# Kernel optimization log

Measured on AMD Instinct MI355X. Metric: run time of the kernel, lower is better.

The kernel has to match this reference:

```python
import jax, jax.numpy as jnp
import numpy as np

RADIUS = 5
KERNEL_SIZE = 2 * RADIUS - 1  # 9
PAD = KERNEL_SIZE // 2        # 4
H, W = 2048, 2048


def make_distance_kernel():
    center = RADIUS - 1
    y, x = jnp.meshgrid(jnp.arange(KERNEL_SIZE), jnp.arange(KERNEL_SIZE), indexing='ij')
    d = jnp.sqrt((x - center).astype(jnp.float32) ** 2 + (y - center).astype(jnp.float32) ** 2)
    return d.at[center, center].set(0.0)


def setup_inputs() -> dict:
    key = jax.random.key(0)
    target = (jax.random.uniform(key, (5, H, W)) < 0.15).astype(jnp.float32)
    distance_kernel = make_distance_kernel()
    return {"target": target, "distance_kernel": distance_kernel}


def _contour_weights(target, kernel):
    combined = (target.sum(axis=0) > 0).astype(jnp.float32)          # [H, W]
    padded = jnp.pad(combined, PAD, mode='edge')                      # replicate pad
    min_d = jnp.full_like(combined, jnp.inf)
    inf = jnp.float32(jnp.inf)
    for i in range(KERNEL_SIZE):
        for j in range(KERNEL_SIZE):
            if i == PAD and j == PAD:
                continue
            shifted = padded[i:i + H, j:j + W]
            diff = (shifted != combined).astype(jnp.float32)
            dist = jnp.where(diff > 0, kernel[i, j] / (diff + 1e-10), inf)
            min_d = jnp.minimum(min_d, dist)
    return jnp.where(min_d < inf, 1.0 / (min_d + 1e-10), 0.0)


def reference(target, distance_kernel):
    feature_weight = target.sum(axis=0)                               # [H, W]
    contour = _contour_weights(target, distance_kernel)
    weights = (feature_weight + contour) ** 2
    weights = (weights - weights.min()) / (weights.max() - weights.min() + 1e-10)
    return weights * (target.sum(axis=0) > 0).astype(jnp.float32)
```

## Files before the change

### kernel.cpp

```cpp
#include <hip/hip_runtime.h>
#include <stdint.h>

#define HH 2048
#define WW 2048
#define NPIX (HH*WW)
#define TS 64
#define NBX (WW/TS)
#define NBY (HH/TS)
#define NBLK (NBX*NBY)
#define HR (TS+8)
#define QW 18
#define BST 24
#define MW 3

__global__ __launch_bounds__(512, 2) void fused_kernel(
    const float* __restrict__ target, const float* __restrict__ dk,
    uint8_t* __restrict__ wcode, float* __restrict__ pmin, float* __restrict__ pmax)
{
    __shared__ uint8_t  bmask[HR * BST];
    __shared__ uint32_t maskw[HR][MW];
    __shared__ uint8_t  lutm2[512];
    __shared__ float    inv_ext[65];
    __shared__ float    redmn[8], redmx[8];

    const int t   = threadIdx.x;
    const int gx0 = blockIdx.x * TS;
    const int gy0 = blockIdx.y * TS;
    const float4* t4 = (const float4*)target;

    {
        uint32_t rev = __builtin_bitreverse32((uint32_t)t) >> 23;
        uint32_t g = ((((uint32_t)t | rev) >> 4) & 0x1Fu) | 0x100u;
        uint32_t mk = (uint32_t)__builtin_ctz(g);
        lutm2[t] = (uint8_t)(mk * mk);
    }
    if (t < 65) inv_ext[t] = 0.0f;
    if (t < HR) {
        uint16_t* p = (uint16_t*)(bmask + t * BST + 18);
        p[0] = 0; p[1] = 0; p[2] = 0;
    }

    const int r  = t >> 3;
    const int xg = t & 7;
    uint32_t fwl, fwh;
    {
        int qb = (gy0 + r) * (WW / 4) + (gx0 >> 2) + xg * 2;
        float4 a0 = t4[qb],                 a1 = t4[qb + 1];
        float4 b0 = t4[qb +     NPIX / 4],  b1 = t4[qb + 1 +     NPIX / 4];
        float4 c0 = t4[qb + 2 * (NPIX/4)],  c1 = t4[qb + 1 + 2 * (NPIX/4)];
        float4 d0 = t4[qb + 3 * (NPIX/4)],  d1 = t4[qb + 1 + 3 * (NPIX/4)];
        float4 e0 = t4[qb + 4 * (NPIX/4)],  e1 = t4[qb + 1 + 4 * (NPIX/4)];
        float f0 = a0.x+b0.x+c0.x+d0.x+e0.x, f1 = a0.y+b0.y+c0.y+d0.y+e0.y;
        float f2 = a0.z+b0.z+c0.z+d0.z+e0.z, f3 = a0.w+b0.w+c0.w+d0.w+e0.w;
        float f4 = a1.x+b1.x+c1.x+d1.x+e1.x, f5 = a1.y+b1.y+c1.y+d1.y+e1.y;
        float f6 = a1.z+b1.z+c1.z+d1.z+e1.z, f7 = a1.w+b1.w+c1.w+d1.w+e1.w;
        fwl = (uint32_t)f0 | ((uint32_t)f1 << 8) | ((uint32_t)f2 << 16) | ((uint32_t)f3 << 24);
        fwh = (uint32_t)f4 | ((uint32_t)f5 << 8) | ((uint32_t)f6 << 16) | ((uint32_t)f7 << 24);
        uint32_t nib0 = (f0!=0.f?1u:0u)|(f1!=0.f?2u:0u)|(f2!=0.f?4u:0u)|(f3!=0.f?8u:0u);
        uint32_t nib1 = (f4!=0.f?1u:0u)|(f5!=0.f?2u:0u)|(f6!=0.f?4u:0u)|(f7!=0.f?8u:0u);
        bmask[(4 + r) * BST + 1 + 2 * xg] = (uint8_t)nib0;
        bmask[(4 + r) * BST + 2 + 2 * xg] = (uint8_t)nib1;
    }

    if (t < 272) {
        int hy, q;
        if (t < 144) { int h = t / QW; q = t - h * QW; hy = (h < 4) ? h : h + 64; }
        else         { int j = t - 144; hy = 4 + (j >> 1); q = (j & 1) ? (QW - 1) : 0; }
        int gy = gy0 - 4 + hy; gy = min(max(gy, 0), HH - 1);
        int col0 = gx0 - 4 + 4 * q;
        int qx = col0 >> 2; qx = min(max(qx, 0), WW / 4 - 1);
        int qb = gy * (WW / 4) + qx;
        float4 a = t4[qb],               b = t4[qb +     NPIX / 4];
        float4 c = t4[qb + 2*(NPIX/4)],  d = t4[qb + 3 * (NPIX/4)];
        float4 e = t4[qb + 4*(NPIX/4)];
        float f0 = a.x+b.x+c.x+d.x+e.x, f1 = a.y+b.y+c.y+d.y+e.y;
        float f2 = a.z+b.z+c.z+d.z+e.z, f3 = a.w+b.w+c.w+d.w+e.w;
        uint32_t nib = (f0!=0.f?1u:0u)|(f1!=0.f?2u:0u)|(f2!=0.f?4u:0u)|(f3!=0.f?8u:0u);
        if (col0 < 0)    nib = (nib & 1u) * 0xFu;
        if (col0 >= WW)  nib = (nib >> 3) * 0xFu;
        bmask[hy * BST + q] = (uint8_t)nib;
    }
    __syncthreads();

    if (t < 81) {
        int iy = t / 9, jx = t - (t / 9) * 9;
        int dy = iy - 4, dx = jx - 4;
        int d2 = dy * dy + dx * dx;
        if (d2 != 0) inv_ext[d2] = 1.0f / (dk[t] / (1.0f + 1e-10f) + 1e-10f);
    }
    if (t < HR * MW) {
        int hy = t / MW, ws = t - (t / MW) * MW;
        uint32_t v0 = *(const uint32_t*)(bmask + hy * BST + 8 * ws);
        uint32_t v1 = *(const uint32_t*)(bmask + hy * BST + 8 * ws + 4);
        v0 = (v0 | (v0 >> 4)) & 0x00FF00FFu; v0 = (v0 | (v0 >> 8)) & 0xFFFFu;
        v1 = (v1 | (v1 >> 4)) & 0x00FF00FFu; v1 = (v1 | (v1 >> 8)) & 0xFFFFu;
        maskw[hy][ws] = v0 | (v1 << 16);
    }
    __syncthreads();

    float lmn = __int_as_float(0x7F800000);
    float lmx = 0.0f;
    {
        const int wsel = xg >> 2;
        const uint32_t sh = (uint32_t)((8 * xg) & 31);
        uint32_t wrow[9];
        #pragma unroll
        for (int k = 0; k < 9; ++k) {
            uint64_t v = (((uint64_t)maskw[r + k][wsel + 1]) << 32) | maskw[r + k][wsel];
            wrow[k] = (uint32_t)(v >> sh);
        }
        uint32_t orx[4], andx[4];
        #pragma unroll
        for (int k = 1; k <= 4; ++k) {
            orx[k-1]  = wrow[4 - k] | wrow[4 + k];
            andx[k-1] = wrow[4 - k] & wrow[4 + k];
        }
        uint32_t outb0 = 0, outb1 = 0;
        #pragma unroll
        for (int j = 0; j < 8; ++j) {
            uint32_t craw = (wrow[4] >> (4 + j)) & 1u;
            uint32_t cm = 0u - craw;
            uint32_t x0 = ((wrow[4] ^ cm) >> j) & 0x1FFu;
            uint32_t d2m = (uint32_t)lutm2[x0];
            #pragma unroll
            for (int k = 1; k <= 4; ++k) {
                uint32_t sel = craw ? andx[k-1] : orx[k-1];
                uint32_t x = ((sel ^ cm) >> j) & 0x1FFu;
                uint32_t d2 = (uint32_t)lutm2[x] + (uint32_t)(k * k);
                d2m = min(d2m, d2);
            }
            float contour = inv_ext[d2m];
            uint32_t enc = (d2m > 32u) ? 26u : d2m;
            uint32_t fwj = (j < 4 ? (fwl >> (8 * j)) : (fwh >> (8 * (j - 4)))) & 0xFFu;
            uint32_t code = ((enc - 1u) << 3) | fwj;
            if (j < 4) outb0 |= code << (8 * j);
            else       outb1 |= code << (8 * (j - 4));
            float wv = (float)fwj + contour;
            wv = wv * wv;
            lmn = fminf(lmn, wv);
            lmx = fmaxf(lmx, wv);
        }
        uint2 ob; ob.x = outb0; ob.y = outb1;
        *(uint2*)(wcode + (gy0 + r) * WW + gx0 + 8 * xg) = ob;
    }

    #pragma unroll
    for (int off = 32; off > 0; off >>= 1) {
        lmn = fminf(lmn, __shfl_xor(lmn, off));
        lmx = fmaxf(lmx, __shfl_xor(lmx, off));
    }
    if ((t & 63) == 0) { redmn[t >> 6] = lmn; redmx[t >> 6] = lmx; }
    __syncthreads();
    if (t == 0) {
        float mn = redmn[0], mx = redmx[0];
        #pragma unroll
        for (int i = 1; i < 8; ++i) { mn = fminf(mn, redmn[i]); mx = fmaxf(mx, redmx[i]); }
        int bid = blockIdx.y * NBX + blockIdx.x;
        pmin[bid] = mn;
        pmax[bid] = mx;
    }
}

__global__ __launch_bounds__(256) void norm_kernel(
    const uint8_t* __restrict__ wcode, const float* __restrict__ dk,
    const float* __restrict__ pmin, const float* __restrict__ pmax,
    float* __restrict__ out)
{
    __shared__ float ct[33];
    __shared__ float wlut[256];
    __shared__ float smn[4], smx[4];
    const int t = threadIdx.x;

    if (t < 33) ct[t] = 0.0f;
    const float4* pn4 = (const float4*)pmin;
    const float4* px4 = (const float4*)pmax;
    float4 a = pn4[t];
    float4 c = px4[t];
    __syncthreads();
    if (t < 81) {
        int iy = t / 9, jx = t - (t / 9) * 9;
        int dy = iy - 4, dx = jx - 4;
        int d2 = dy * dy + dx * dx;
        if (d2 != 0) ct[d2] = 1.0f / (dk[t] / (1.0f + 1e-10f) + 1e-10f);
    }
    __syncthreads();
    {
        float wv = (float)(t & 7) + ct[(t >> 3) + 1];
        wlut[t] = wv * wv;
    }
    float mn = fminf(fminf(a.x, a.y), fminf(a.z, a.w));
    float mx = fmaxf(fmaxf(c.x, c.y), fmaxf(c.z, c.w));
    #pragma unroll
    for (int off = 32; off > 0; off >>= 1) {
        mn = fminf(mn, __shfl_xor(mn, off));
        mx = fmaxf(mx, __shfl_xor(mx, off));
    }
    if ((t & 63) == 0) { smn[t >> 6] = mn; smx[t >> 6] = mx; }
    __syncthreads();
    mn = fminf(fminf(smn[0], smn[1]), fminf(smn[2], smn[3]));
    mx = fmaxf(fmaxf(smx[0], smx[1]), fmaxf(smx[2], smx[3]));
    const float rden = 1.0f / (mx - mn + 1e-10f);

    const int i = blockIdx.x * 256 + t;
    uint2 cb = ((const uint2*)wcode)[i];
    uint32_t b0 = cb.x, b1 = cb.y;
    float4 o0, o1;
    o0.x = (b0 & 7u)         ? (wlut[b0 & 0xFFu] - mn) * rden         : 0.0f;
    o0.y = ((b0 >> 8) & 7u)  ? (wlut[(b0 >> 8) & 0xFFu] - mn) * rden  : 0.0f;
    o0.z = ((b0 >> 16) & 7u) ? (wlut[(b0 >> 16) & 0xFFu] - mn) * rden : 0.0f;
    o0.w = ((b0 >> 24) & 7u) ? (wlut[b0 >> 24] - mn) * rden           : 0.0f;
    o1.x = (b1 & 7u)         ? (wlut[b1 & 0xFFu] - mn) * rden         : 0.0f;
    o1.y = ((b1 >> 8) & 7u)  ? (wlut[(b1 >> 8) & 0xFFu] - mn) * rden  : 0.0f;
    o1.z = ((b1 >> 16) & 7u) ? (wlut[(b1 >> 16) & 0xFFu] - mn) * rden : 0.0f;
    o1.w = ((b1 >> 24) & 7u) ? (wlut[b1 >> 24] - mn) * rden           : 0.0f;
    ((float4*)out)[i * 2]     = o0;
    ((float4*)out)[i * 2 + 1] = o1;
}

extern "C" void kernel_launch(void* const* d_in, const int* in_sizes, int n_in,
                              void* d_out, int out_size, void* d_ws, size_t ws_size,
                              hipStream_t stream)
{
    const float* target = (const float*)d_in[0];
    const float* dk     = (const float*)d_in[1];
    float* out = (float*)d_out;

    uint8_t* wsb = (uint8_t*)d_ws;
    uint8_t* wcode = wsb;
    float*   pmin  = (float*)(wsb + NPIX);
    float*   pmax  = pmin + NBLK;

    fused_kernel<<<dim3(NBX, NBY), 512, 0, stream>>>(target, dk, wcode, pmin, pmax);

    norm_kernel<<<NPIX / 8 / 256, 256, 0, stream>>>(wcode, dk, pmin, pmax, out);
}
```

Measured before the change: 39.61 us.

## Process two tiles per block and prefetch the second tile's loads

Each block now handles two horizontally adjacent 64x64 tiles, which halves the grid to 512 blocks. The global loads for the second tile are issued into registers while the first tile is still being computed, so memory latency overlaps with the stencil work. Block setup (LUTs, inverse distances) is also amortized over two tiles. The risks are higher register pressure from holding the prefetched float4s and fewer blocks to cover the CUs, which could lower occupancy and load balance.

```diff
diff --git a/kernel.cpp b/kernel.cpp
--- a/kernel.cpp
+++ b/kernel.cpp
@@ -5,63 +5,29 @@
 #define WW 2048
 #define NPIX (HH*WW)
 #define TS 64
-#define NBX (WW/TS)
-#define NBY (HH/TS)
-#define NBLK (NBX*NBY)
+#define NBPX 16
+#define NBY 32
+#define NBLK (NBPX*NBY)
 #define HR (TS+8)
 #define QW 18
 #define BST 24
 #define MW 3
 
-__global__ __launch_bounds__(512, 2) void fused_kernel(
-    const float* __restrict__ target, const float* __restrict__ dk,
-    uint8_t* __restrict__ wcode, float* __restrict__ pmin, float* __restrict__ pmax)
-{
-    __shared__ uint8_t  bmask[HR * BST];
-    __shared__ uint32_t maskw[HR][MW];
-    __shared__ uint8_t  lutm2[512];
-    __shared__ float    inv_ext[65];
-    __shared__ float    redmn[8], redmx[8];
-
-    const int t   = threadIdx.x;
-    const int gx0 = blockIdx.x * TS;
-    const int gy0 = blockIdx.y * TS;
-    const float4* t4 = (const float4*)target;
-
-    {
-        uint32_t rev = __builtin_bitreverse32((uint32_t)t) >> 23;
-        uint32_t g = ((((uint32_t)t | rev) >> 4) & 0x1Fu) | 0x100u;
-        uint32_t mk = (uint32_t)__builtin_ctz(g);
-        lutm2[t] = (uint8_t)(mk * mk);
-    }
-    if (t < 65) inv_ext[t] = 0.0f;
-    if (t < HR) {
-        uint16_t* p = (uint16_t*)(bmask + t * BST + 18);
-        p[0] = 0; p[1] = 0; p[2] = 0;
-    }
-
-    const int r  = t >> 3;
-    const int xg = t & 7;
-    uint32_t fwl, fwh;
-    {
-        int qb = (gy0 + r) * (WW / 4) + (gx0 >> 2) + xg * 2;
-        float4 a0 = t4[qb],                 a1 = t4[qb + 1];
-        float4 b0 = t4[qb +     NPIX / 4],  b1 = t4[qb + 1 +     NPIX / 4];
-        float4 c0 = t4[qb + 2 * (NPIX/4)],  c1 = t4[qb + 1 + 2 * (NPIX/4)];
-        float4 d0 = t4[qb + 3 * (NPIX/4)],  d1 = t4[qb + 1 + 3 * (NPIX/4)];
-        float4 e0 = t4[qb + 4 * (NPIX/4)],  e1 = t4[qb + 1 + 4 * (NPIX/4)];
-        float f0 = a0.x+b0.x+c0.x+d0.x+e0.x, f1 = a0.y+b0.y+c0.y+d0.y+e0.y;
-        float f2 = a0.z+b0.z+c0.z+d0.z+e0.z, f3 = a0.w+b0.w+c0.w+d0.w+e0.w;
-        float f4 = a1.x+b1.x+c1.x+d1.x+e1.x, f5 = a1.y+b1.y+c1.y+d1.y+e1.y;
-        float f6 = a1.z+b1.z+c1.z+d1.z+e1.z, f7 = a1.w+b1.w+c1.w+d1.w+e1.w;
-        fwl = (uint32_t)f0 | ((uint32_t)f1 << 8) | ((uint32_t)f2 << 16) | ((uint32_t)f3 << 24);
-        fwh = (uint32_t)f4 | ((uint32_t)f5 << 8) | ((uint32_t)f6 << 16) | ((uint32_t)f7 << 24);
-        uint32_t nib0 = (f0!=0.f?1u:0u)|(f1!=0.f?2u:0u)|(f2!=0.f?4u:0u)|(f3!=0.f?8u:0u);
-        uint32_t nib1 = (f4!=0.f?1u:0u)|(f5!=0.f?2u:0u)|(f6!=0.f?4u:0u)|(f7!=0.f?8u:0u);
-        bmask[(4 + r) * BST + 1 + 2 * xg] = (uint8_t)nib0;
-        bmask[(4 + r) * BST + 2 + 2 * xg] = (uint8_t)nib1;
-    }
-
+struct Loads {
+    float4 a0,a1,b0,b1,c0,c1,d0,d1,e0,e1;
+    float4 ra,rb,rc,rd,re;
+    int col0;
+};
+
+__device__ __forceinline__ void issue_tile(const float4* __restrict__ t4,
+    int gx0, int gy0, int t, int r, int xg, Loads& L)
+{
+    int qb = (gy0 + r) * (WW / 4) + (gx0 >> 2) + xg * 2;
+    L.a0 = t4[qb];                   L.a1 = t4[qb + 1];
+    L.b0 = t4[qb + NPIX/4];          L.b1 = t4[qb + 1 + NPIX/4];
+    L.c0 = t4[qb + 2*(NPIX/4)];      L.c1 = t4[qb + 1 + 2*(NPIX/4)];
+    L.d0 = t4[qb + 3*(NPIX/4)];      L.d1 = t4[qb + 1 + 3*(NPIX/4)];
+    L.e0 = t4[qb + 4*(NPIX/4)];      L.e1 = t4[qb + 1 + 4*(NPIX/4)];
     if (t < 272) {
         int hy, q;
         if (t < 144) { int h = t / QW; q = t - h * QW; hy = (h < 4) ? h : h + 64; }
@@ -69,38 +35,99 @@
         int gy = gy0 - 4 + hy; gy = min(max(gy, 0), HH - 1);
         int col0 = gx0 - 4 + 4 * q;
         int qx = col0 >> 2; qx = min(max(qx, 0), WW / 4 - 1);
-        int qb = gy * (WW / 4) + qx;
-        float4 a = t4[qb],               b = t4[qb +     NPIX / 4];
-        float4 c = t4[qb + 2*(NPIX/4)],  d = t4[qb + 3 * (NPIX/4)];
-        float4 e = t4[qb + 4*(NPIX/4)];
-        float f0 = a.x+b.x+c.x+d.x+e.x, f1 = a.y+b.y+c.y+d.y+e.y;
-        float f2 = a.z+b.z+c.z+d.z+e.z, f3 = a.w+b.w+c.w+d.w+e.w;
-        uint32_t nib = (f0!=0.f?1u:0u)|(f1!=0.f?2u:0u)|(f2!=0.f?4u:0u)|(f3!=0.f?8u:0u);
-        if (col0 < 0)    nib = (nib & 1u) * 0xFu;
-        if (col0 >= WW)  nib = (nib >> 3) * 0xFu;
+        int rqb = gy * (WW / 4) + qx;
+        L.ra = t4[rqb];               L.rb = t4[rqb + NPIX/4];
+        L.rc = t4[rqb + 2*(NPIX/4)];  L.rd = t4[rqb + 3*(NPIX/4)];
+        L.re = t4[rqb + 4*(NPIX/4)];
+        L.col0 = col0;
+    }
+}
+
+__device__ __forceinline__ void pack_tile(uint8_t* bmask, int t, int r, int xg,
+    const Loads& L, uint32_t& fwl, uint32_t& fwh)
+{
+    float f0 = L.a0.x+L.b0.x+L.c0.x+L.d0.x+L.e0.x, f1 = L.a0.y+L.b0.y+L.c0.y+L.d0.y+L.e0.y;
+    float f2 = L.a0.z+L.b0.z+L.c0.z+L.d0.z+L.e0.z, f3 = L.a0.w+L.b0.w+L.c0.w+L.d0.w+L.e0.w;
+    float f4 = L.a1.x+L.b1.x+L.c1.x+L.d1.x+L.e1.x, f5 = L.a1.y+L.b1.y+L.c1.y+L.d1.y+L.e1.y;
+    float f6 = L.a1.z+L.b1.z+L.c1.z+L.d1.z+L.e1.z, f7 = L.a1.w+L.b1.w+L.c1.w+L.d1.w+L.e1.w;
+    fwl = (uint32_t)f0 | ((uint32_t)f1 << 8) | ((uint32_t)f2 << 16) | ((uint32_t)f3 << 24);
+    fwh = (uint32_t)f4 | ((uint32_t)f5 << 8) | ((uint32_t)f6 << 16) | ((uint32_t)f7 << 24);
+    uint32_t nib0 = (f0!=0.f?1u:0u)|(f1!=0.f?2u:0u)|(f2!=0.f?4u:0u)|(f3!=0.f?8u:0u);
+    uint32_t nib1 = (f4!=0.f?1u:0u)|(f5!=0.f?2u:0u)|(f6!=0.f?4u:0u)|(f7!=0.f?8u:0u);
+    bmask[(4 + r) * BST + 1 + 2 * xg] = (uint8_t)nib0;
+    bmask[(4 + r) * BST + 2 + 2 * xg] = (uint8_t)nib1;
+    if (t < 272) {
+        int hy, q;
+        if (t < 144) { int h = t / QW; q = t - h * QW; hy = (h < 4) ? h : h + 64; }
+        else         { int j = t - 144; hy = 4 + (j >> 1); q = (j & 1) ? (QW - 1) : 0; }
+        float g0 = L.ra.x+L.rb.x+L.rc.x+L.rd.x+L.re.x, g1 = L.ra.y+L.rb.y+L.rc.y+L.rd.y+L.re.y;
+        float g2 = L.ra.z+L.rb.z+L.rc.z+L.rd.z+L.re.z, g3 = L.ra.w+L.rb.w+L.rc.w+L.rd.w+L.re.w;
+        uint32_t nib = (g0!=0.f?1u:0u)|(g1!=0.f?2u:0u)|(g2!=0.f?4u:0u)|(g3!=0.f?8u:0u);
+        if (L.col0 < 0)    nib = (nib & 1u) * 0xFu;
+        if (L.col0 >= WW)  nib = (nib >> 3) * 0xFu;
         bmask[hy * BST + q] = (uint8_t)nib;
     }
-    __syncthreads();
-
-    if (t < 81) {
-        int iy = t / 9, jx = t - (t / 9) * 9;
-        int dy = iy - 4, dx = jx - 4;
-        int d2 = dy * dy + dx * dx;
-        if (d2 != 0) inv_ext[d2] = 1.0f / (dk[t] / (1.0f + 1e-10f) + 1e-10f);
-    }
-    if (t < HR * MW) {
-        int hy = t / MW, ws = t - (t / MW) * MW;
-        uint32_t v0 = *(const uint32_t*)(bmask + hy * BST + 8 * ws);
-        uint32_t v1 = *(const uint32_t*)(bmask + hy * BST + 8 * ws + 4);
-        v0 = (v0 | (v0 >> 4)) & 0x00FF00FFu; v0 = (v0 | (v0 >> 8)) & 0xFFFFu;
-        v1 = (v1 | (v1 >> 4)) & 0x00FF00FFu; v1 = (v1 | (v1 >> 8)) & 0xFFFFu;
-        maskw[hy][ws] = v0 | (v1 << 16);
-    }
-    __syncthreads();
-
+}
+
+__global__ __launch_bounds__(512, 2) void fused_kernel(
+    const float* __restrict__ target, const float* __restrict__ dk,
+    uint8_t* __restrict__ wcode, float* __restrict__ pmin, float* __restrict__ pmax)
+{
+    __shared__ uint8_t  bmask[HR * BST];
+    __shared__ uint32_t maskw[HR][MW];
+    __shared__ uint8_t  lutm2[512];
+    __shared__ float    inv_ext[65];
+    __shared__ float    redmn[8], redmx[8];
+
+    const int t   = threadIdx.x;
+    const int gy0 = blockIdx.y * TS;
+    const int gxA = (2 * blockIdx.x) * TS;
+    const int gxB = gxA + TS;
+    const float4* t4 = (const float4*)target;
+    const int r  = t >> 3;
+    const int xg = t & 7;
+
+    Loads L;
+    issue_tile(t4, gxA, gy0, t, r, xg, L);
+
+    {
+        uint32_t rev = __builtin_bitreverse32((uint32_t)t) >> 23;
+        uint32_t g = ((((uint32_t)t | rev) >> 4) & 0x1Fu) | 0x100u;
+        lutm2[t] = (uint8_t)(__builtin_ctz(g) * __builtin_ctz(g));
+    }
+    if (t < 65) inv_ext[t] = 0.0f;
+    if (t < HR) {
+        uint16_t* p = (uint16_t*)(bmask + t * BST + 18);
+        p[0] = 0; p[1] = 0; p[2] = 0;
+    }
+
+    uint32_t fwl, fwh;
     float lmn = __int_as_float(0x7F800000);
     float lmx = 0.0f;
-    {
+
+    #pragma unroll
+    for (int it = 0; it < 2; ++it) {
+        const int gx0 = it ? gxB : gxA;
+        pack_tile(bmask, t, r, xg, L, fwl, fwh);
+        __syncthreads();
+        if (it == 0 && t < 81) {
+            int iy = t / 9, jx = t - (t / 9) * 9;
+            int dy = iy - 4, dx = jx - 4;
+            int d2 = dy * dy + dx * dx;
+            if (d2 != 0) inv_ext[d2] = 1.0f / (dk[t] / (1.0f + 1e-10f) + 1e-10f);
+        }
+        if (t < HR * MW) {
+            int hy = t / MW, ws = t - (t / MW) * MW;
+            uint32_t v0 = *(const uint32_t*)(bmask + hy * BST + 8 * ws);
+            uint32_t v1 = *(const uint32_t*)(bmask + hy * BST + 8 * ws + 4);
+            v0 = (v0 | (v0 >> 4)) & 0x00FF00FFu; v0 = (v0 | (v0 >> 8)) & 0xFFFFu;
+            v1 = (v1 | (v1 >> 4)) & 0x00FF00FFu; v1 = (v1 | (v1 >> 8)) & 0xFFFFu;
+            maskw[hy][ws] = v0 | (v1 << 16);
+        }
+        __syncthreads();
+        if (it == 0)
+            issue_tile(t4, gxB, gy0, t, r, xg, L);
+
         const int wsel = xg >> 2;
         const uint32_t sh = (uint32_t)((8 * xg) & 31);
         uint32_t wrow[9];
@@ -155,7 +182,7 @@
         float mn = redmn[0], mx = redmx[0];
         #pragma unroll
         for (int i = 1; i < 8; ++i) { mn = fminf(mn, redmn[i]); mx = fmaxf(mx, redmx[i]); }
-        int bid = blockIdx.y * NBX + blockIdx.x;
+        int bid = blockIdx.y * NBPX + blockIdx.x;
         pmin[bid] = mn;
         pmax[bid] = mx;
     }
@@ -172,10 +199,8 @@
     const int t = threadIdx.x;
 
     if (t < 33) ct[t] = 0.0f;
-    const float4* pn4 = (const float4*)pmin;
-    const float4* px4 = (const float4*)pmax;
-    float4 a = pn4[t];
-    float4 c = px4[t];
+    float mn0 = fminf(pmin[t], pmin[t + 256]);
+    float mx0 = fmaxf(pmax[t], pmax[t + 256]);
     __syncthreads();
     if (t < 81) {
         int iy = t / 9, jx = t - (t / 9) * 9;
@@ -188,8 +213,7 @@
         float wv = (float)(t & 7) + ct[(t >> 3) + 1];
         wlut[t] = wv * wv;
     }
-    float mn = fminf(fminf(a.x, a.y), fminf(a.z, a.w));
-    float mx = fmaxf(fmaxf(c.x, c.y), fmaxf(c.z, c.w));
+    float mn = mn0, mx = mx0;
     #pragma unroll
     for (int off = 32; off > 0; off >>= 1) {
         mn = fminf(mn, __shfl_xor(mn, off));
@@ -230,7 +254,7 @@
     float*   pmin  = (float*)(wsb + NPIX);
     float*   pmax  = pmin + NBLK;
 
-    fused_kernel<<<dim3(NBX, NBY), 512, 0, stream>>>(target, dk, wcode, pmin, pmax);
+    fused_kernel<<<dim3(NBPX, NBY), 512, 0, stream>>>(target, dk, wcode, pmin, pmax);
 
     norm_kernel<<<NPIX / 8 / 256, 256, 0, stream>>>(wcode, dk, pmin, pmax, out);
 }
```

Result: no change. 40.23 us (+1.6%).
